# Kernel tuning notes

Hardware: AMD Instinct MI355X
Metric: run time of the kernel (lower is better)

The kernel has to match this reference:

```python
import jax, jax.numpy as jnp
import numpy as np

B, L, D, H = 2, 2048, 1024, 16
HD = D // H  # head dim = 64


def setup_inputs() -> dict:
    key = jax.random.key(0)
    ks = jax.random.split(key, 5)
    s = 1.0 / np.sqrt(D)
    return {
        "x": jax.random.normal(ks[0], (B, L, D), dtype=jnp.float32),
        "mask": jnp.ones((B, 1, 1, L), dtype=jnp.int32),
        "Wq": jax.random.normal(ks[1], (D, D), dtype=jnp.float32) * s,
        "bq": jnp.zeros((D,), dtype=jnp.float32),
        "Wk": jax.random.normal(ks[2], (D, D), dtype=jnp.float32) * s,
        "bk": jnp.zeros((D,), dtype=jnp.float32),
        "Wv": jax.random.normal(ks[3], (D, D), dtype=jnp.float32) * s,
        "bv": jnp.zeros((D,), dtype=jnp.float32),
        "Wo": jax.random.normal(ks[4], (D, D), dtype=jnp.float32) * s,
        "bo": jnp.zeros((D,), dtype=jnp.float32),
    }


def reference(x, mask, Wq, bq, Wk, bk, Wv, bv, Wo, bo):
    Bx, Lx = x.shape[0], x.shape[1]
    # torch nn.Linear: y = x @ W.T + b
    q = (jnp.einsum("bld,ed->ble", x, Wq) + bq).reshape(Bx, Lx, H, HD).transpose(0, 2, 1, 3)
    k = (jnp.einsum("bld,ed->ble", x, Wk) + bk).reshape(Bx, Lx, H, HD).transpose(0, 2, 1, 3)
    v = (jnp.einsum("bld,ed->ble", x, Wv) + bv).reshape(Bx, Lx, H, HD).transpose(0, 2, 1, 3)
    # [B, H, L, L] scores
    scores = jnp.einsum("bhqd,bhkd->bhqk", q, k) / np.sqrt(HD).astype(np.float32)
    # faithful to original: masked positions are set to the tiny value 1e-9 (not -inf)
    scores = jnp.where(mask == 0, jnp.float32(1e-9), scores)
    attn = jax.nn.softmax(scores, axis=-1)
    # dropout_prob=0.0 -> identity (eval mode)
    out = jnp.einsum("bhqk,bhkd->bhqd", attn, v)  # [B, H, L, HD]
    out = out.transpose(0, 2, 1, 3).reshape(Bx, Lx, D)
    return jnp.einsum("bld,ed->ble", out, Wo) + bo
```

## Files before the change

### kernel.cpp

```cpp
#include <hip/hip_runtime.h>
#include <hip/hip_bf16.h>

typedef _Float16 f16;
typedef _Float16 f16x8 __attribute__((ext_vector_type(8)));
typedef _Float16 f16x4 __attribute__((ext_vector_type(4)));
typedef float f32x4 __attribute__((ext_vector_type(4)));

#define LDS_LOAD16(gptr, lptr)                                                             \
  __builtin_amdgcn_global_load_lds(                                                        \
      (const __attribute__((address_space(1))) unsigned int*)(gptr),                       \
      (__attribute__((address_space(3))) unsigned int*)(lptr), 16, 0, 0)

#define ALPHA 0.18033688f

__global__ __launch_bounds__(256) void conv_all(const float* __restrict__ x,
                                                const float* __restrict__ Wq,
                                                const float* __restrict__ Wk,
                                                const float* __restrict__ Wv,
                                                const float* __restrict__ Wo,
                                                f16* __restrict__ xh, f16* __restrict__ wqh,
                                                f16* __restrict__ wkh, f16* __restrict__ wvh,
                                                f16* __restrict__ woh) {
  int i = blockIdx.x * 256 + threadIdx.x;
  const float* src;
  f16* dst;
  int off;
  if (i < 524288) {
    src = x; dst = xh; off = i;
  } else {
    int j = i - 524288;
    int w = j >> 17;
    off = j & 131071;
    src = (w == 0) ? Wq : (w == 1) ? Wk : (w == 2) ? Wv : Wo;
    dst = (w == 0) ? wqh : (w == 1) ? wkh : (w == 2) ? wvh : woh;
  }
  const float4* s4 = (const float4*)src;
  float4 a = s4[2 * off];
  float4 b = s4[2 * off + 1];
  f16x8 o = {(f16)a.x, (f16)a.y, (f16)a.z, (f16)a.w,
             (f16)b.x, (f16)b.y, (f16)b.z, (f16)b.w};
  *(f16x8*)(dst + (size_t)off * 8) = o;
}

__global__ __launch_bounds__(256) void gemm_qkv(const f16* __restrict__ A,
                                                const f16* __restrict__ W0,
                                                const f16* __restrict__ W1,
                                                const f16* __restrict__ W2,
                                                const float* __restrict__ b0,
                                                const float* __restrict__ b1,
                                                const float* __restrict__ b2,
                                                f16* __restrict__ qo, f16* __restrict__ ko,
                                                f16* __restrict__ vo) {
  constexpr int K = 1024, BM = 128, BK = 32;
  __shared__ f16 aT[BM * BK];
  __shared__ f16 bT[BM * BK];
  const int z = blockIdx.z;
  const f16* Bw = (z == 0) ? W0 : (z == 1) ? W1 : W2;
  const float* bias = (z == 0) ? b0 : (z == 1) ? b1 : b2;
  const int tid = threadIdx.x, wid = tid >> 6, lane = tid & 63;
  const int mb = blockIdx.y * BM, nb = blockIdx.x * BM;
  const int wr = wid >> 1, wc = wid & 1;
  const int lr = lane & 15, hi = lane >> 4;

  f32x4 acc[4][4] = {};

  const int r0 = tid >> 2, s0 = tid & 3;
  const int ci1 = 256 + tid, r1 = ci1 >> 2, s1 = ci1 & 3;

  for (int kt = 0; kt < K / BK; ++kt) {
    __syncthreads();
    const int kb = kt * BK;
    LDS_LOAD16(A + (size_t)(mb + r0) * K + kb + s0 * 8, (char*)aT + wid * 1024);
    LDS_LOAD16(Bw + (size_t)(nb + r0) * K + kb + s0 * 8, (char*)bT + wid * 1024);
    LDS_LOAD16(A + (size_t)(mb + r1) * K + kb + s1 * 8, (char*)aT + 4096 + wid * 1024);
    LDS_LOAD16(Bw + (size_t)(nb + r1) * K + kb + s1 * 8, (char*)bT + 4096 + wid * 1024);
    __syncthreads();

    f16x8 af[4], bf[4];
#pragma unroll
    for (int i = 0; i < 4; ++i) af[i] = *(const f16x8*)&aT[(wr * 64 + i * 16 + lr) * BK + hi * 8];
#pragma unroll
    for (int j = 0; j < 4; ++j) bf[j] = *(const f16x8*)&bT[(wc * 64 + j * 16 + lr) * BK + hi * 8];
    __builtin_amdgcn_s_setprio(1);
#pragma unroll
    for (int i = 0; i < 4; ++i)
#pragma unroll
      for (int j = 0; j < 4; ++j)
        acc[i][j] = __builtin_amdgcn_mfma_f32_16x16x32_f16(af[i], bf[j], acc[i][j], 0, 0, 0);
    __builtin_amdgcn_s_setprio(0);
  }

  const float scale = (z == 0) ? ALPHA : 1.0f;
#pragma unroll
  for (int i = 0; i < 4; ++i) {
#pragma unroll
    for (int j = 0; j < 4; ++j) {
      const int row = mb + wr * 64 + i * 16 + hi * 4;
      const int col = nb + wc * 64 + j * 16 + lr;
      const float bv = bias[col];
      const int hh = col >> 6, dd = col & 63;
      if (z == 2) {
        const int bb = row >> 11, l = row & 2047;
        f16x4 v4;
#pragma unroll
        for (int r = 0; r < 4; ++r) v4[r] = (f16)(acc[i][j][r] + bv);
        *(f16x4*)(vo + ((((size_t)bb * 16 + hh) * 64 + dd) * 2048 + l)) = v4;
      } else {
        f16* o = z ? ko : qo;
#pragma unroll
        for (int r = 0; r < 4; ++r) {
          const int m2 = row + r;
          const int bb = m2 >> 11, l = m2 & 2047;
          o[((((size_t)bb * 16 + hh) * 2048 + l) * 64) + dd] = (f16)((acc[i][j][r] + bv) * scale);
        }
      }
    }
  }
}

__global__ __launch_bounds__(256) void gemm_o(const f16* __restrict__ A,
                                              const f16* __restrict__ W,
                                              const float* __restrict__ bias,
                                              float* __restrict__ out) {
  constexpr int K = 1024, N = 1024, BK = 32;
  __shared__ f16 aT[64 * BK];
  __shared__ f16 bT[128 * BK];
  const int tid = threadIdx.x, wid = tid >> 6, lane = tid & 63;
  const int lr = lane & 15, hi = lane >> 4;
  const int mb = blockIdx.y * 64, nb = blockIdx.x * 128;
  const int wr = wid >> 1, wc = wid & 1;
  f32x4 acc[2][4] = {};
  const int ra = tid >> 2, sa = tid & 3;
  const int rb1 = (256 + tid) >> 2, sb1 = (256 + tid) & 3;

  for (int kt = 0; kt < K / BK; ++kt) {
    __syncthreads();
    const int kb = kt * BK;
    LDS_LOAD16(A + (size_t)(mb + ra) * K + kb + sa * 8, (char*)aT + wid * 1024);
    LDS_LOAD16(W + (size_t)(nb + ra) * K + kb + sa * 8, (char*)bT + wid * 1024);
    LDS_LOAD16(W + (size_t)(nb + rb1) * K + kb + sb1 * 8, (char*)bT + 4096 + wid * 1024);
    __syncthreads();
    f16x8 af[2], bf[4];
#pragma unroll
    for (int i = 0; i < 2; ++i) af[i] = *(const f16x8*)&aT[(wr * 32 + i * 16 + lr) * BK + hi * 8];
#pragma unroll
    for (int j = 0; j < 4; ++j) bf[j] = *(const f16x8*)&bT[(wc * 64 + j * 16 + lr) * BK + hi * 8];
    __builtin_amdgcn_s_setprio(1);
#pragma unroll
    for (int i = 0; i < 2; ++i)
#pragma unroll
      for (int j = 0; j < 4; ++j)
        acc[i][j] = __builtin_amdgcn_mfma_f32_16x16x32_f16(af[i], bf[j], acc[i][j], 0, 0, 0);
    __builtin_amdgcn_s_setprio(0);
  }
#pragma unroll
  for (int i = 0; i < 2; ++i)
#pragma unroll
    for (int j = 0; j < 4; ++j) {
      const int col = nb + wc * 64 + j * 16 + lr;
      const float bv = bias[col];
#pragma unroll
      for (int r = 0; r < 4; ++r)
        out[(size_t)(mb + wr * 32 + i * 16 + hi * 4 + r) * N + col] = acc[i][j][r] + bv;
    }
}

__global__ __launch_bounds__(256) void attn128(const f16* __restrict__ Qh,
                                               const f16* __restrict__ Kh,
                                               const f16* __restrict__ Vt,
                                               const int* __restrict__ mask,
                                               f16* __restrict__ Oa) {
  constexpr int L = 2048, HD = 64, H = 16;
  __shared__ f16 kT[2][64 * 64];
  __shared__ f16 vT[2][64 * 64];
  __shared__ f16 pT[4][32 * 64];

  const int tid = threadIdx.x, wid = tid >> 6, lane = tid & 63;
  const int bh = blockIdx.y, b = bh >> 4, h = bh & 15;
  const int lr = lane & 15, hi = lane >> 4;
  const int sw = lr & 7;

  const f16* Qb = Qh + (size_t)bh * L * HD;
  const f16* Kb = Kh + (size_t)bh * L * HD;
  const f16* Vb = Vt + (size_t)bh * HD * L;
  const int* mrow = mask + b * L;

  const int qr0 = blockIdx.x * 128 + wid * 32;
  f16x8 qf[2][2];
#pragma unroll
  for (int qg = 0; qg < 2; ++qg)
#pragma unroll
    for (int kh = 0; kh < 2; ++kh)
      qf[qg][kh] = *(const f16x8*)&Qb[(size_t)(qr0 + qg * 16 + lr) * HD + kh * 32 + hi * 8];

  f32x4 oacc[2][4] = {};
  float lsum[2][4] = {};

  const int kr0 = tid >> 3, ks0 = (tid & 7) ^ (kr0 & 7);
  const int ci1 = 256 + tid, kr1 = ci1 >> 3, ks1 = (ci1 & 7) ^ (kr1 & 7);
  char* pTb = (char*)pT + wid * 4096;

#define STAGE(bb, kt)                                                                        \
  do {                                                                                       \
    LDS_LOAD16(Kb + (size_t)((kt) * 64 + kr0) * HD + ks0 * 8,                                \
               (char*)kT + (bb) * 8192 + wid * 1024);                                        \
    LDS_LOAD16(Vb + (size_t)kr0 * L + (kt) * 64 + ks0 * 8,                                   \
               (char*)vT + (bb) * 8192 + wid * 1024);                                        \
    LDS_LOAD16(Kb + (size_t)((kt) * 64 + kr1) * HD + ks1 * 8,                                \
               (char*)kT + (bb) * 8192 + 4096 + wid * 1024);                                 \
    LDS_LOAD16(Vb + (size_t)kr1 * L + (kt) * 64 + ks1 * 8,                                   \
               (char*)vT + (bb) * 8192 + 4096 + wid * 1024);                                 \
  } while (0)

  STAGE(0, 0);
  __syncthreads();
  int buf = 0;

  for (int kt = 0; kt < L / 64; ++kt) {
    if (kt + 1 < L / 64) STAGE(buf ^ 1, kt + 1);
    const char* kB = (char*)kT + buf * 8192;
    const char* vB = (char*)vT + buf * 8192;

    f16x8 kf[4][2];
#pragma unroll
    for (int nf = 0; nf < 4; ++nf)
#pragma unroll
      for (int k2 = 0; k2 < 2; ++k2)
        kf[nf][k2] = *(const f16x8*)(kB + (nf * 16 + lr) * 128 + ((k2 * 4 + hi) ^ sw) * 16);

    f32x4 s[2][4];
    __builtin_amdgcn_s_setprio(1);
#pragma unroll
    for (int qg = 0; qg < 2; ++qg)
#pragma unroll
      for (int nf = 0; nf < 4; ++nf) {
        f32x4 z = {-8.f, -8.f, -8.f, -8.f};
        z = __builtin_amdgcn_mfma_f32_16x16x32_f16(qf[qg][0], kf[nf][0], z, 0, 0, 0);
        z = __builtin_amdgcn_mfma_f32_16x16x32_f16(qf[qg][1], kf[nf][1], z, 0, 0, 0);
        s[qg][nf] = z;
      }
    __builtin_amdgcn_s_setprio(0);

#pragma unroll
    for (int nf = 0; nf < 4; ++nf) {
      const int mv = mrow[kt * 64 + nf * 16 + lr];
#pragma unroll
      for (int qg = 0; qg < 2; ++qg)
#pragma unroll
        for (int r = 0; r < 4; ++r) {
          float t = mv ? s[qg][nf][r] : (1.44269504e-9f - 8.0f);
          float p = __builtin_amdgcn_exp2f(t);
          lsum[qg][r] += p;
          const int row = qg * 16 + hi * 4 + r;
          *(f16*)(pTb + row * 128 + ((nf * 32 + lr * 2) ^ ((row & 7) << 4))) = (f16)p;
        }
    }

    f16x8 pf[2][2];
#pragma unroll
    for (int qg = 0; qg < 2; ++qg)
#pragma unroll
      for (int k2 = 0; k2 < 2; ++k2)
        pf[qg][k2] = *(const f16x8*)(pTb + (qg * 16 + lr) * 128 + ((k2 * 4 + hi) ^ sw) * 16);
    __builtin_amdgcn_s_setprio(1);
#pragma unroll
    for (int k2 = 0; k2 < 2; ++k2)
#pragma unroll
      for (int df = 0; df < 4; ++df) {
        f16x8 vf = *(const f16x8*)(vB + (df * 16 + lr) * 128 + ((k2 * 4 + hi) ^ sw) * 16);
        oacc[0][df] = __builtin_amdgcn_mfma_f32_16x16x32_f16(pf[0][k2], vf, oacc[0][df], 0, 0, 0);
        oacc[1][df] = __builtin_amdgcn_mfma_f32_16x16x32_f16(pf[1][k2], vf, oacc[1][df], 0, 0, 0);
      }
    __builtin_amdgcn_s_setprio(0);

    __syncthreads();
    buf ^= 1;
  }

#pragma unroll
  for (int qg = 0; qg < 2; ++qg)
#pragma unroll
    for (int r = 0; r < 4; ++r) {
      float t = lsum[qg][r];
      t += __shfl_xor(t, 1);
      t += __shfl_xor(t, 2);
      t += __shfl_xor(t, 4);
      t += __shfl_xor(t, 8);
      lsum[qg][r] = 1.0f / t;
    }
#pragma unroll
  for (int qg = 0; qg < 2; ++qg)
#pragma unroll
    for (int df = 0; df < 4; ++df)
#pragma unroll
      for (int r = 0; r < 4; ++r) {
        const int l = qr0 + qg * 16 + hi * 4 + r;
        Oa[(((size_t)b * L + l) * H + h) * HD + df * 16 + lr] =
            (f16)(oacc[qg][df][r] * lsum[qg][r]);
      }
}

extern "C" void kernel_launch(void* const* d_in, const int* in_sizes, int n_in,
                              void* d_out, int out_size, void* d_ws, size_t ws_size,
                              hipStream_t stream) {
  const float* x  = (const float*)d_in[0];
  const int* mask = (const int*)d_in[1];
  const float* Wq = (const float*)d_in[2];
  const float* bq = (const float*)d_in[3];
  const float* Wk = (const float*)d_in[4];
  const float* bk = (const float*)d_in[5];
  const float* Wv = (const float*)d_in[6];
  const float* bv = (const float*)d_in[7];
  const float* Wo = (const float*)d_in[8];
  const float* bo = (const float*)d_in[9];
  float* out = (float*)d_out;

  char* ws = (char*)d_ws;
  const size_t MB = 1u << 20;
  f16* xh  = (f16*)(ws);
  f16* wqh = (f16*)(ws + 8 * MB);
  f16* wkh = (f16*)(ws + 10 * MB);
  f16* wvh = (f16*)(ws + 12 * MB);
  f16* woh = (f16*)(ws + 14 * MB);
  f16* qh  = (f16*)(ws + 16 * MB);
  f16* kh  = (f16*)(ws + 24 * MB);
  f16* vth = (f16*)(ws + 32 * MB);
  f16* oah = (f16*)(ws + 40 * MB);

  conv_all<<<4096, 256, 0, stream>>>(x, Wq, Wk, Wv, Wo, xh, wqh, wkh, wvh, woh);

  gemm_qkv<<<dim3(8, 32, 3), 256, 0, stream>>>(xh, wqh, wkh, wvh, bq, bk, bv, qh, kh, vth);

  attn128<<<dim3(16, 32), 256, 0, stream>>>(qh, kh, vth, mask, oah);

  gemm_o<<<dim3(8, 64), 256, 0, stream>>>(oah, woh, bo, out);
}
```

Measured before the change: 136.7 us.

## Replace 4-wave attention block with single-wave 64-row blocks without barriers

The attention kernel moves from 256-thread blocks (4 waves × 32 query rows) to 64-thread single-wave blocks that each handle 64 query rows, which removes __syncthreads in favour of explicit vmcnt/lgkmcnt waits. The QK^T MFMA is transposed so each lane holds four consecutive keys for one query row. That allows vectorized int4 mask loads and f16x4 P stores to LDS, and reduces the row-sum to two cross-lane shuffles. A head-interleaved block mapping is added for L2 locality, at the cost of each wave staging its own K/V tiles with 16 outstanding loads and using a larger per-wave LDS footprint.

```diff
diff --git a/kernel.cpp b/kernel.cpp
--- a/kernel.cpp
+++ b/kernel.cpp
@@ -12,6 +12,7 @@
       (__attribute__((address_space(3))) unsigned int*)(lptr), 16, 0, 0)
 
 #define ALPHA 0.18033688f
+#define MASKVAL (1.44269504e-9f - 8.0f)
 
 __global__ __launch_bounds__(256) void conv_all(const float* __restrict__ x,
                                                 const float* __restrict__ Wq,
@@ -165,139 +166,149 @@
     }
 }
 
-__global__ __launch_bounds__(256) void attn128(const f16* __restrict__ Qh,
-                                               const f16* __restrict__ Kh,
-                                               const f16* __restrict__ Vt,
-                                               const int* __restrict__ mask,
-                                               f16* __restrict__ Oa) {
-  constexpr int L = 2048, HD = 64, H = 16;
+__global__ __launch_bounds__(64) void attn1w(const f16* __restrict__ Qh,
+                                             const f16* __restrict__ Kh,
+                                             const f16* __restrict__ Vt,
+                                             const int* __restrict__ mask,
+                                             f16* __restrict__ Oa) {
+  constexpr int L = 2048, HD = 64, H = 16, NT = L / 64;
   __shared__ f16 kT[2][64 * 64];
   __shared__ f16 vT[2][64 * 64];
-  __shared__ f16 pT[4][32 * 64];
-
-  const int tid = threadIdx.x, wid = tid >> 6, lane = tid & 63;
-  const int bh = blockIdx.y, b = bh >> 4, h = bh & 15;
+  __shared__ f16 pT[64 * 64];
+
+  const int lane = threadIdx.x;
   const int lr = lane & 15, hi = lane >> 4;
   const int sw = lr & 7;
 
-  const f16* Qb = Qh + (size_t)bh * L * HD;
-  const f16* Kb = Kh + (size_t)bh * L * HD;
-  const f16* Vb = Vt + (size_t)bh * HD * L;
+  const int bid = blockIdx.x;
+  const int head = (bid & 7) * 4 + ((bid >> 3) >> 5);
+  const int qb = (bid >> 3) & 31;
+  const int b = head >> 4, h = head & 15;
+  const int qr0 = qb * 64;
+
+  const f16* Qb = Qh + (size_t)head * L * HD;
+  const f16* Kb = Kh + (size_t)head * L * HD;
+  const f16* Vb = Vt + (size_t)head * HD * L;
   const int* mrow = mask + b * L;
 
-  const int qr0 = blockIdx.x * 128 + wid * 32;
-  f16x8 qf[2][2];
-#pragma unroll
-  for (int qg = 0; qg < 2; ++qg)
-#pragma unroll
-    for (int kh = 0; kh < 2; ++kh)
-      qf[qg][kh] = *(const f16x8*)&Qb[(size_t)(qr0 + qg * 16 + lr) * HD + kh * 32 + hi * 8];
-
-  f32x4 oacc[2][4] = {};
-  float lsum[2][4] = {};
-
-  const int kr0 = tid >> 3, ks0 = (tid & 7) ^ (kr0 & 7);
-  const int ci1 = 256 + tid, kr1 = ci1 >> 3, ks1 = (ci1 & 7) ^ (kr1 & 7);
-  char* pTb = (char*)pT + wid * 4096;
-
-#define STAGE(bb, kt)                                                                        \
-  do {                                                                                       \
-    LDS_LOAD16(Kb + (size_t)((kt) * 64 + kr0) * HD + ks0 * 8,                                \
-               (char*)kT + (bb) * 8192 + wid * 1024);                                        \
-    LDS_LOAD16(Vb + (size_t)kr0 * L + (kt) * 64 + ks0 * 8,                                   \
-               (char*)vT + (bb) * 8192 + wid * 1024);                                        \
-    LDS_LOAD16(Kb + (size_t)((kt) * 64 + kr1) * HD + ks1 * 8,                                \
-               (char*)kT + (bb) * 8192 + 4096 + wid * 1024);                                 \
-    LDS_LOAD16(Vb + (size_t)kr1 * L + (kt) * 64 + ks1 * 8,                                   \
-               (char*)vT + (bb) * 8192 + 4096 + wid * 1024);                                 \
-  } while (0)
-
-  STAGE(0, 0);
-  __syncthreads();
+  const int srow = lane >> 3;
+  const int schk = (lane & 7) ^ (srow & 7);
+  const int kOffL = srow * HD + schk * 8;
+  const int vOffL = srow * L + schk * 8;
+  char* kTb = (char*)kT;
+  char* vTb = (char*)vT;
+  char* pTb = (char*)pT;
+
+#define STAGE1W(bb, kt)                                                                     \
+  _Pragma("unroll") for (int c = 0; c < 8; ++c) {                                           \
+    LDS_LOAD16(Kb + (size_t)((kt) * 64 + c * 8) * HD + kOffL, kTb + (bb) * 8192 + c * 1024);\
+    LDS_LOAD16(Vb + (size_t)(c * 8) * L + (kt) * 64 + vOffL, vTb + (bb) * 8192 + c * 1024); \
+  }
+
+  f16x8 qf[4][2];
+#pragma unroll
+  for (int qg = 0; qg < 4; ++qg)
+#pragma unroll
+    for (int k2 = 0; k2 < 2; ++k2)
+      qf[qg][k2] = *(const f16x8*)&Qb[(size_t)(qr0 + qg * 16 + lr) * HD + k2 * 32 + hi * 8];
+
+  f32x4 oacc[4][4] = {};
+  float lsum[4] = {0.f, 0.f, 0.f, 0.f};
+
+  STAGE1W(0, 0);
   int buf = 0;
 
-  for (int kt = 0; kt < L / 64; ++kt) {
-    if (kt + 1 < L / 64) STAGE(buf ^ 1, kt + 1);
-    const char* kB = (char*)kT + buf * 8192;
-    const char* vB = (char*)vT + buf * 8192;
+  for (int kt = 0; kt < NT; ++kt) {
+    if (kt + 1 < NT) {
+      STAGE1W(buf ^ 1, kt + 1);
+      asm volatile("s_waitcnt vmcnt(16)" ::: "memory");
+    } else {
+      asm volatile("s_waitcnt vmcnt(0)" ::: "memory");
+    }
+    __builtin_amdgcn_sched_barrier(0);
+    const char* kB = kTb + buf * 8192;
+    const char* vB = vTb + buf * 8192;
+
+    int4 mv[4];
+#pragma unroll
+    for (int nf = 0; nf < 4; ++nf) mv[nf] = *(const int4*)&mrow[kt * 64 + nf * 16 + hi * 4];
 
     f16x8 kf[4][2];
 #pragma unroll
     for (int nf = 0; nf < 4; ++nf)
 #pragma unroll
       for (int k2 = 0; k2 < 2; ++k2)
-        kf[nf][k2] = *(const f16x8*)(kB + (nf * 16 + lr) * 128 + ((k2 * 4 + hi) ^ sw) * 16);
-
-    f32x4 s[2][4];
-    __builtin_amdgcn_s_setprio(1);
-#pragma unroll
-    for (int qg = 0; qg < 2; ++qg)
+        kf[nf][k2] = *(const f16x8*)(kB + (nf * 16 + lr) * 128 + (((k2 * 4 + hi) ^ sw) * 16));
+
+#pragma unroll
+    for (int qg = 0; qg < 4; ++qg) {
+      f32x4 s[4];
+      __builtin_amdgcn_s_setprio(1);
 #pragma unroll
       for (int nf = 0; nf < 4; ++nf) {
         f32x4 z = {-8.f, -8.f, -8.f, -8.f};
-        z = __builtin_amdgcn_mfma_f32_16x16x32_f16(qf[qg][0], kf[nf][0], z, 0, 0, 0);
-        z = __builtin_amdgcn_mfma_f32_16x16x32_f16(qf[qg][1], kf[nf][1], z, 0, 0, 0);
-        s[qg][nf] = z;
+        z = __builtin_amdgcn_mfma_f32_16x16x32_f16(kf[nf][0], qf[qg][0], z, 0, 0, 0);
+        z = __builtin_amdgcn_mfma_f32_16x16x32_f16(kf[nf][1], qf[qg][1], z, 0, 0, 0);
+        s[nf] = z;
+      }
+      __builtin_amdgcn_s_setprio(0);
+#pragma unroll
+      for (int nf = 0; nf < 4; ++nf) {
+        float p0 = __builtin_amdgcn_exp2f(mv[nf].x ? s[nf][0] : MASKVAL);
+        float p1 = __builtin_amdgcn_exp2f(mv[nf].y ? s[nf][1] : MASKVAL);
+        float p2 = __builtin_amdgcn_exp2f(mv[nf].z ? s[nf][2] : MASKVAL);
+        float p3 = __builtin_amdgcn_exp2f(mv[nf].w ? s[nf][3] : MASKVAL);
+        lsum[qg] += (p0 + p1) + (p2 + p3);
+        f16x4 pw = {(f16)p0, (f16)p1, (f16)p2, (f16)p3};
+        *(f16x4*)(pTb + (qg * 16 + lr) * 128 + ((nf * 32 + hi * 8) ^ (sw << 4))) = pw;
+      }
+    }
+
+    asm volatile("s_waitcnt lgkmcnt(0)" ::: "memory");
+    __builtin_amdgcn_sched_barrier(0);
+
+    f16x8 pf[4][2];
+#pragma unroll
+    for (int qg = 0; qg < 4; ++qg)
+#pragma unroll
+      for (int k2 = 0; k2 < 2; ++k2)
+        pf[qg][k2] = *(const f16x8*)(pTb + (qg * 16 + lr) * 128 + (((k2 * 4 + hi) ^ sw) * 16));
+    __builtin_amdgcn_s_setprio(1);
+#pragma unroll
+    for (int k2 = 0; k2 < 2; ++k2)
+#pragma unroll
+      for (int df = 0; df < 4; ++df) {
+        f16x8 vf = *(const f16x8*)(vB + (df * 16 + lr) * 128 + (((k2 * 4 + hi) ^ sw) * 16));
+#pragma unroll
+        for (int qg = 0; qg < 4; ++qg)
+          oacc[qg][df] = __builtin_amdgcn_mfma_f32_16x16x32_f16(pf[qg][k2], vf, oacc[qg][df], 0, 0, 0);
       }
     __builtin_amdgcn_s_setprio(0);
 
-#pragma unroll
-    for (int nf = 0; nf < 4; ++nf) {
-      const int mv = mrow[kt * 64 + nf * 16 + lr];
-#pragma unroll
-      for (int qg = 0; qg < 2; ++qg)
-#pragma unroll
-        for (int r = 0; r < 4; ++r) {
-          float t = mv ? s[qg][nf][r] : (1.44269504e-9f - 8.0f);
-          float p = __builtin_amdgcn_exp2f(t);
-          lsum[qg][r] += p;
-          const int row = qg * 16 + hi * 4 + r;
-          *(f16*)(pTb + row * 128 + ((nf * 32 + lr * 2) ^ ((row & 7) << 4))) = (f16)p;
-        }
-    }
-
-    f16x8 pf[2][2];
-#pragma unroll
-    for (int qg = 0; qg < 2; ++qg)
-#pragma unroll
-      for (int k2 = 0; k2 < 2; ++k2)
-        pf[qg][k2] = *(const f16x8*)(pTb + (qg * 16 + lr) * 128 + ((k2 * 4 + hi) ^ sw) * 16);
-    __builtin_amdgcn_s_setprio(1);
-#pragma unroll
-    for (int k2 = 0; k2 < 2; ++k2)
-#pragma unroll
-      for (int df = 0; df < 4; ++df) {
-        f16x8 vf = *(const f16x8*)(vB + (df * 16 + lr) * 128 + ((k2 * 4 + hi) ^ sw) * 16);
-        oacc[0][df] = __builtin_amdgcn_mfma_f32_16x16x32_f16(pf[0][k2], vf, oacc[0][df], 0, 0, 0);
-        oacc[1][df] = __builtin_amdgcn_mfma_f32_16x16x32_f16(pf[1][k2], vf, oacc[1][df], 0, 0, 0);
-      }
-    __builtin_amdgcn_s_setprio(0);
-
-    __syncthreads();
     buf ^= 1;
   }
 
-#pragma unroll
-  for (int qg = 0; qg < 2; ++qg)
-#pragma unroll
-    for (int r = 0; r < 4; ++r) {
-      float t = lsum[qg][r];
-      t += __shfl_xor(t, 1);
-      t += __shfl_xor(t, 2);
-      t += __shfl_xor(t, 4);
-      t += __shfl_xor(t, 8);
-      lsum[qg][r] = 1.0f / t;
-    }
-#pragma unroll
-  for (int qg = 0; qg < 2; ++qg)
+  float linv[4];
+#pragma unroll
+  for (int qg = 0; qg < 4; ++qg) {
+    float t = lsum[qg];
+    t += __shfl_xor(t, 16);
+    t += __shfl_xor(t, 32);
+    linv[qg] = 1.0f / t;
+  }
+#pragma unroll
+  for (int qg = 0; qg < 4; ++qg) {
+    float rinv[4];
+#pragma unroll
+    for (int r = 0; r < 4; ++r) rinv[r] = __shfl(linv[qg], hi * 4 + r);
 #pragma unroll
     for (int df = 0; df < 4; ++df)
 #pragma unroll
       for (int r = 0; r < 4; ++r) {
         const int l = qr0 + qg * 16 + hi * 4 + r;
-        Oa[(((size_t)b * L + l) * H + h) * HD + df * 16 + lr] =
-            (f16)(oacc[qg][df][r] * lsum[qg][r]);
-      }
+        Oa[(((size_t)b * L + l) * H + h) * HD + df * 16 + lr] = (f16)(oacc[qg][df][r] * rinv[r]);
+      }
+  }
 }
 
 extern "C" void kernel_launch(void* const* d_in, const int* in_sizes, int n_in,
@@ -331,7 +342,7 @@
 
   gemm_qkv<<<dim3(8, 32, 3), 256, 0, stream>>>(xh, wqh, wkh, wvh, bq, bk, bv, qh, kh, vth);
 
-  attn128<<<dim3(16, 32), 256, 0, stream>>>(qh, kh, vth, mask, oah);
+  attn1w<<<dim3(1024), 64, 0, stream>>>(qh, kh, vth, mask, oah);
 
   gemm_o<<<dim3(8, 64), 256, 0, stream>>>(oah, woh, bo, out);
 }
```

Result: no change. 135.1 us (-1.2%).
